# Performance work log

Hardware: AMD Instinct MI355X
Metric: run time of the kernel (lower is better)

## Reference

```python
import jax, jax.numpy as jnp
import numpy as np

NUM_HEADS = 16
FIELD_SIZE = 512
SIGMA = 3.0
EMB = 1024


def _causal_kernel_fft(G, sigma):
    # kernel[i] = exp(-|i - G//2| / sigma) for i < G//2, else 0; normalized
    i = np.arange(G)
    dist = np.abs(i - G // 2)
    kernel = np.where(i >= G // 2, 0.0, np.exp(-dist / sigma)).astype(np.float32)
    kernel = kernel / (kernel.sum() + 1e-8)
    return jnp.asarray(np.fft.rfft(kernel), dtype=jnp.complex64)


def setup_inputs() -> dict:
    key = jax.random.key(0)
    ks = jax.random.split(key, 9)
    B, N, D = 4, 4096, EMB
    s = 1.0 / np.sqrt(D)
    return {
        "x": jax.random.normal(ks[0], (B, N, D), dtype=jnp.float32),
        "q_w": jax.random.uniform(ks[1], (D, D), minval=-s, maxval=s, dtype=jnp.float32),
        "q_b": jnp.zeros((D,), jnp.float32),
        "k_w": jax.random.uniform(ks[2], (D, D), minval=-s, maxval=s, dtype=jnp.float32),
        "k_b": jnp.zeros((D,), jnp.float32),
        "v_w": jax.random.uniform(ks[3], (D, D), minval=-s, maxval=s, dtype=jnp.float32),
        "v_b": jnp.zeros((D,), jnp.float32),
        "out_w": jax.random.uniform(ks[4], (D, D), minval=-s, maxval=s, dtype=jnp.float32),
        "out_b": jnp.zeros((D,), jnp.float32),
    }


def reference(x, q_w, q_b, k_w, k_b, v_w, v_b, out_w, out_b):
    B, N, D = x.shape
    H, hd, G = NUM_HEADS, D // NUM_HEADS, FIELD_SIZE

    # projections (q is computed in the original but unused downstream)
    q = x @ q_w.T + q_b  # noqa: F841 (faithful to original)
    k = (x @ k_w.T + k_b).reshape(B, N, H, hd).transpose(0, 2, 1, 3)  # (B,H,N,hd)
    v = (x @ v_w.T + v_b).reshape(B, N, H, hd).transpose(0, 2, 1, 3)

    # map sequence positions -> field bins (same for all b, h)
    pos = jnp.arange(N, dtype=jnp.float32) / max(N - 1, 1) * (G - 1)
    field_idx = jnp.clip(pos.astype(jnp.int32), 0, G - 1)  # (N,)

    # weighted values by key magnitude
    k_mag = jnp.linalg.norm(k, axis=-1, keepdims=True)  # (B,H,N,1)
    wv = v * k_mag  # (B,H,N,hd)

    # scatter-add tokens into field bins (vectorized over B,H,hd)
    field = jax.ops.segment_sum(wv.transpose(2, 0, 1, 3), field_idx,
                                num_segments=G)  # (G,B,H,hd)
    field = field.transpose(1, 2, 0, 3)  # (B,H,G,hd)

    # causal convolution along the field via FFT (circular, as in original)
    kfft = _causal_kernel_fft(G, SIGMA)
    f_fft = jnp.fft.rfft(field, n=G, axis=2)
    conv = jnp.fft.irfft(f_fft * kfft[None, None, :, None], n=G, axis=2)

    # gather back to token positions
    out = conv[:, :, field_idx, :]  # (B,H,N,hd)
    out = out.transpose(0, 2, 1, 3).reshape(B, N, D)
    return out @ out_w.T + out_b
```

## Files before the change

### kernel.cpp

```cpp
#include <hip/hip_runtime.h>
#include <hip/hip_bf16.h>

#define NPOS 4096
#define DIM  1024
#define GSZ  512

#define GAS __attribute__((address_space(1)))
#define LAS __attribute__((address_space(3)))

typedef __attribute__((ext_vector_type(8))) short bf16x8;
typedef __attribute__((ext_vector_type(4))) float f32x4;

__device__ __forceinline__ void async_load16(const void* g, void* l) {
  __builtin_amdgcn_global_load_lds((const GAS void*)g, (LAS void*)l, 16, 0, 0);
}

__device__ __forceinline__ int fidx_of(int n) {
  return (int)(((float)n / 4095.0f) * 511.0f);
}

__device__ __forceinline__ float bf2f(unsigned short s) {
  union { unsigned u; float f; } v; v.u = ((unsigned)s) << 16; return v.f;
}

__device__ __forceinline__ void bin_range(int g, int& i0, int& i1) {
  i0 = (g * 4095 + 510) / 511;
  while (i0 > 0 && fidx_of(i0 - 1) >= g) --i0;
  while (i0 < NPOS && fidx_of(i0) < g) ++i0;
  if (g == GSZ - 1) { i1 = NPOS; return; }
  i1 = ((g + 1) * 4095 + 510) / 511;
  while (i1 > 0 && fidx_of(i1 - 1) >= g + 1) --i1;
  while (i1 < NPOS && fidx_of(i1) < g + 1) ++i1;
}

__global__ __launch_bounds__(256) void cast_all(
    const float* __restrict__ x, const float* __restrict__ kw,
    const float* __restrict__ vw, const float* __restrict__ ow,
    __hip_bfloat16* __restrict__ xb, __hip_bfloat16* __restrict__ kvwb,
    __hip_bfloat16* __restrict__ outwb) {
  int blk = blockIdx.x;
  const float* src; __hip_bfloat16* dst; int off;
  if (blk < 16384)      { src = x;  dst = xb;              off = blk; }
  else if (blk < 17408) { src = kw; dst = kvwb;            off = blk - 16384; }
  else if (blk < 18432) { src = vw; dst = kvwb + 1048576;  off = blk - 17408; }
  else                  { src = ow; dst = outwb;           off = blk - 18432; }
  int i = (off * 256 + threadIdx.x) * 4;
  float4 f = *(const float4*)(src + i);
  ushort4 o;
  __hip_bfloat16 t;
  t = __float2bfloat16(f.x); o.x = *(unsigned short*)&t;
  t = __float2bfloat16(f.y); o.y = *(unsigned short*)&t;
  t = __float2bfloat16(f.z); o.z = *(unsigned short*)&t;
  t = __float2bfloat16(f.w); o.w = *(unsigned short*)&t;
  *(ushort4*)(dst + i) = o;
}

__global__ __launch_bounds__(256) void gemm_bt(
    const __hip_bfloat16* __restrict__ A,
    const __hip_bfloat16* __restrict__ B,
    const float* __restrict__ bias0, const float* __restrict__ bias1,
    __hip_bfloat16* __restrict__ C, int N) {
  const int K = 1024;
  __shared__ __align__(16) __hip_bfloat16 As[128 * 32];
  __shared__ __align__(16) __hip_bfloat16 Bs[128 * 32];
  const int tid = threadIdx.x;
  const int bm = blockIdx.x * 128, bn = blockIdx.y * 128;

  const int srow = tid >> 2;
  const int scol = (tid & 3) * 8;
  const __hip_bfloat16* ap0 = A + (size_t)(bm + srow) * K + scol;
  const __hip_bfloat16* ap1 = A + (size_t)(bm + srow + 64) * K + scol;
  const __hip_bfloat16* bp0 = B + (size_t)(bn + srow) * K + scol;
  const __hip_bfloat16* bp1 = B + (size_t)(bn + srow + 64) * K + scol;
  __hip_bfloat16* as0 = &As[srow * 32 + scol];
  __hip_bfloat16* as1 = &As[(srow + 64) * 32 + scol];
  __hip_bfloat16* bs0 = &Bs[srow * 32 + scol];
  __hip_bfloat16* bs1 = &Bs[(srow + 64) * 32 + scol];

  const int wave = tid >> 6, lane = tid & 63;
  const int wm = (wave >> 1) * 64, wn = (wave & 1) * 64;
  const int m16 = lane & 15, quad = lane >> 4;

  f32x4 acc[4][4];
#pragma unroll
  for (int i = 0; i < 4; i++)
#pragma unroll
    for (int j = 0; j < 4; j++) acc[i][j] = (f32x4)0.f;

  for (int k0 = 0; k0 < K; k0 += 32) {
    async_load16(ap0 + k0, as0);
    async_load16(ap1 + k0, as1);
    async_load16(bp0 + k0, bs0);
    async_load16(bp1 + k0, bs1);
    __syncthreads();
    bf16x8 af[4], bfr[4];
#pragma unroll
    for (int mt = 0; mt < 4; mt++)
      af[mt] = *(const bf16x8*)&As[(wm + mt * 16 + m16) * 32 + quad * 8];
#pragma unroll
    for (int nt = 0; nt < 4; nt++)
      bfr[nt] = *(const bf16x8*)&Bs[(wn + nt * 16 + m16) * 32 + quad * 8];
#pragma unroll
    for (int mt = 0; mt < 4; mt++)
#pragma unroll
      for (int nt = 0; nt < 4; nt++)
        acc[mt][nt] = __builtin_amdgcn_mfma_f32_16x16x32_bf16(af[mt], bfr[nt], acc[mt][nt], 0, 0, 0);
    __syncthreads();
  }

#pragma unroll
  for (int mt = 0; mt < 4; mt++) {
#pragma unroll
    for (int nt = 0; nt < 4; nt++) {
      int col = bn + wn + nt * 16 + m16;
      float bv = (col < 1024) ? bias0[col] : bias1[col - 1024];
#pragma unroll
      for (int r = 0; r < 4; r++) {
        int row = bm + wm + mt * 16 + quad * 4 + r;
        C[(size_t)row * N + col] = __float2bfloat16(acc[mt][nt][r] + bv);
      }
    }
  }
}

__global__ __launch_bounds__(256) void gemm_out_bcast(
    const __hip_bfloat16* __restrict__ A,
    const __hip_bfloat16* __restrict__ B,
    const float* __restrict__ bias,
    float* __restrict__ out) {
  const int K = 1024;
  __shared__ __align__(16) __hip_bfloat16 As[64 * 32];
  __shared__ __align__(16) __hip_bfloat16 Bs[128 * 32];
  const int tid = threadIdx.x;
  const int bm = blockIdx.x * 64, bn = blockIdx.y * 128;

  const int srow = tid >> 2;
  const int scol = (tid & 3) * 8;
  const __hip_bfloat16* ap0 = A + (size_t)(bm + srow) * K + scol;
  const __hip_bfloat16* bp0 = B + (size_t)(bn + srow) * K + scol;
  const __hip_bfloat16* bp1 = B + (size_t)(bn + srow + 64) * K + scol;
  __hip_bfloat16* as0 = &As[srow * 32 + scol];
  __hip_bfloat16* bs0 = &Bs[srow * 32 + scol];
  __hip_bfloat16* bs1 = &Bs[(srow + 64) * 32 + scol];

  const int wave = tid >> 6, lane = tid & 63;
  const int wm = (wave >> 1) * 32, wn = (wave & 1) * 64;
  const int m16 = lane & 15, quad = lane >> 4;

  f32x4 acc[2][4];
#pragma unroll
  for (int i = 0; i < 2; i++)
#pragma unroll
    for (int j = 0; j < 4; j++) acc[i][j] = (f32x4)0.f;

  for (int k0 = 0; k0 < K; k0 += 32) {
    async_load16(ap0 + k0, as0);
    async_load16(bp0 + k0, bs0);
    async_load16(bp1 + k0, bs1);
    __syncthreads();
    bf16x8 af[2], bfr[4];
#pragma unroll
    for (int mt = 0; mt < 2; mt++)
      af[mt] = *(const bf16x8*)&As[(wm + mt * 16 + m16) * 32 + quad * 8];
#pragma unroll
    for (int nt = 0; nt < 4; nt++)
      bfr[nt] = *(const bf16x8*)&Bs[(wn + nt * 16 + m16) * 32 + quad * 8];
#pragma unroll
    for (int mt = 0; mt < 2; mt++)
#pragma unroll
      for (int nt = 0; nt < 4; nt++)
        acc[mt][nt] = __builtin_amdgcn_mfma_f32_16x16x32_bf16(af[mt], bfr[nt], acc[mt][nt], 0, 0, 0);
    __syncthreads();
  }

  float bv[4];
#pragma unroll
  for (int nt = 0; nt < 4; nt++) bv[nt] = bias[bn + wn + nt * 16 + m16];

#pragma unroll
  for (int mt = 0; mt < 2; mt++) {
#pragma unroll
    for (int r = 0; r < 4; r++) {
      int row = bm + wm + mt * 16 + quad * 4 + r;
      int b = row >> 9, g = row & (GSZ - 1);
      int i0, i1;
      bin_range(g, i0, i1);
      float v0 = acc[mt][0][r] + bv[0];
      float v1 = acc[mt][1][r] + bv[1];
      float v2 = acc[mt][2][r] + bv[2];
      float v3 = acc[mt][3][r] + bv[3];
      for (int n = i0; n < i1; ++n) {
        float* orow = out + ((size_t)(b * NPOS + n)) * DIM + bn + wn + m16;
        orow[0]  = v0;
        orow[16] = v1;
        orow[32] = v2;
        orow[48] = v3;
      }
    }
  }
}

__global__ __launch_bounds__(256) void wv_field_kernel(
    const __hip_bfloat16* __restrict__ KV, float* __restrict__ field) {
  const int b = blockIdx.x, g = blockIdx.y;
  int i0, i1;
  bin_range(g, i0, i1);
  int cnt = i1 - i0;
  if (cnt > 12) cnt = 12;
  __shared__ float km[12][16];
  const int tid = threadIdx.x;
  if (tid < cnt * 16) {
    int r = tid >> 4, h = tid & 15;
    const unsigned short* kp = (const unsigned short*)KV + (size_t)(b * NPOS + i0 + r) * 2048 + h * 64;
    float s = 0.f;
#pragma unroll
    for (int e = 0; e < 64; e += 8) {
      bf16x8 v = *(const bf16x8*)(kp + e);
#pragma unroll
      for (int q = 0; q < 8; ++q) { float f = bf2f((unsigned short)v[q]); s += f * f; }
    }
    km[r][h] = sqrtf(s);
  }
  __syncthreads();
  if (tid < 128) {
    int c0 = tid * 8, h = c0 >> 6;
    float acc[8] = {0.f, 0.f, 0.f, 0.f, 0.f, 0.f, 0.f, 0.f};
    for (int r = 0; r < cnt; ++r) {
      float w = km[r][h];
      bf16x8 v = *(const bf16x8*)((const unsigned short*)KV + (size_t)(b * NPOS + i0 + r) * 2048 + 1024 + c0);
#pragma unroll
      for (int q = 0; q < 8; ++q) acc[q] += w * bf2f((unsigned short)v[q]);
    }
    float4* fp = (float4*)(field + ((size_t)(b * GSZ + g)) * DIM + c0);
    fp[0] = make_float4(acc[0], acc[1], acc[2], acc[3]);
    fp[1] = make_float4(acc[4], acc[5], acc[6], acc[7]);
  }
}

__global__ __launch_bounds__(256) void conv_ema_kernel(
    const float* __restrict__ field, __hip_bfloat16* __restrict__ convb) {
  const int b = blockIdx.x, h = blockIdx.y;
  const int tid = threadIdx.x;
  const int c = tid & 63;
  const int chunk = blockIdx.z * 4 + (tid >> 6);
  const int n0 = chunk * 64;
  const float a = expf(-1.0f / 3.0f);
  const float w1 = 1.0f - a;
  const float* fb = field + (size_t)b * GSZ * DIM + h * 64 + c;
  float acc = 0.f;
#pragma unroll 4
  for (int n = n0 + 127; n >= n0 + 64; --n) {
    float f = fb[(size_t)((n + 257) & (GSZ - 1)) * DIM];
    acc = w1 * f + a * acc;
  }
#pragma unroll 4
  for (int n = n0 + 63; n >= n0; --n) {
    float f = fb[(size_t)((n + 257) & (GSZ - 1)) * DIM];
    acc = w1 * f + a * acc;
    convb[((size_t)(b * GSZ) + n) * DIM + h * 64 + c] = __float2bfloat16(acc);
  }
}

extern "C" void kernel_launch(void* const* d_in, const int* in_sizes, int n_in,
                              void* d_out, int out_size, void* d_ws, size_t ws_size,
                              hipStream_t stream) {
  (void)in_sizes; (void)n_in; (void)out_size; (void)ws_size;
  const float* x     = (const float*)d_in[0];
  const float* k_w   = (const float*)d_in[3];
  const float* k_b   = (const float*)d_in[4];
  const float* v_w   = (const float*)d_in[5];
  const float* v_b   = (const float*)d_in[6];
  const float* out_w = (const float*)d_in[7];
  const float* out_b = (const float*)d_in[8];

  char* p = (char*)d_ws;
  __hip_bfloat16* xb    = (__hip_bfloat16*)p; p += (size_t)16384 * 1024 * 2;
  __hip_bfloat16* kvwb  = (__hip_bfloat16*)p; p += (size_t)2048 * 1024 * 2;
  __hip_bfloat16* outwb = (__hip_bfloat16*)p; p += (size_t)1024 * 1024 * 2;
  __hip_bfloat16* KV    = (__hip_bfloat16*)p; p += (size_t)16384 * 2048 * 2;
  float*          field = (float*)p;          p += (size_t)4 * 512 * 1024 * 4;
  __hip_bfloat16* convb = (__hip_bfloat16*)p;

  cast_all<<<19456, 256, 0, stream>>>(x, k_w, v_w, out_w, xb, kvwb, outwb);

  gemm_bt<<<dim3(128, 16), 256, 0, stream>>>(xb, kvwb, k_b, v_b, KV, 2048);

  wv_field_kernel<<<dim3(4, 512), 256, 0, stream>>>(KV, field);
  conv_ema_kernel<<<dim3(4, 16, 2), 256, 0, stream>>>(field, convb);

  gemm_out_bcast<<<dim3(32, 8), 256, 0, stream>>>(convb, outwb, out_b, (float*)d_out);
}
```

Measured before the change: 283.5 us.

## Stage conv field slab in LDS and coalesce broadcast output writes via LDS

The causal EMA convolution kernel now loads a 192-row slab of the field into shared memory with float4 loads and runs its recurrence from LDS. The grid doubles to 128-row chunks, each using 64 rows of warm-up per 32-row sub-chunk. The output GEMM stages its result tile in LDS and then writes each broadcast output row with fully coalesced float4 stores, where it previously issued strided scalar stores per MFMA lane. This targets the write bandwidth of the large 64MB output, at the cost of extra LDS traffic and a barrier.

```diff
diff --git a/kernel.cpp b/kernel.cpp
--- a/kernel.cpp
+++ b/kernel.cpp
@@ -123,14 +123,80 @@
   }
 }
 
+__global__ __launch_bounds__(256) void wv_field_kernel(
+    const __hip_bfloat16* __restrict__ KV, float* __restrict__ field) {
+  const int b = blockIdx.x, g = blockIdx.y;
+  int i0, i1;
+  bin_range(g, i0, i1);
+  int cnt = i1 - i0;
+  if (cnt > 12) cnt = 12;
+  __shared__ float km[12][16];
+  const int tid = threadIdx.x;
+  if (tid < cnt * 16) {
+    int r = tid >> 4, h = tid & 15;
+    const unsigned short* kp = (const unsigned short*)KV + (size_t)(b * NPOS + i0 + r) * 2048 + h * 64;
+    float s = 0.f;
+#pragma unroll
+    for (int e = 0; e < 64; e += 8) {
+      bf16x8 v = *(const bf16x8*)(kp + e);
+#pragma unroll
+      for (int q = 0; q < 8; ++q) { float f = bf2f((unsigned short)v[q]); s += f * f; }
+    }
+    km[r][h] = sqrtf(s);
+  }
+  __syncthreads();
+  if (tid < 128) {
+    int c0 = tid * 8, h = c0 >> 6;
+    float acc[8] = {0.f, 0.f, 0.f, 0.f, 0.f, 0.f, 0.f, 0.f};
+    for (int r = 0; r < cnt; ++r) {
+      float w = km[r][h];
+      bf16x8 v = *(const bf16x8*)((const unsigned short*)KV + (size_t)(b * NPOS + i0 + r) * 2048 + 1024 + c0);
+#pragma unroll
+      for (int q = 0; q < 8; ++q) acc[q] += w * bf2f((unsigned short)v[q]);
+    }
+    float4* fp = (float4*)(field + ((size_t)(b * GSZ + g)) * DIM + c0);
+    fp[0] = make_float4(acc[0], acc[1], acc[2], acc[3]);
+    fp[1] = make_float4(acc[4], acc[5], acc[6], acc[7]);
+  }
+}
+
+__global__ __launch_bounds__(256) void conv_ema_kernel(
+    const float* __restrict__ field, __hip_bfloat16* __restrict__ convb) {
+  const int b = blockIdx.x, h = blockIdx.y, n0 = blockIdx.z * 128;
+  __shared__ float slab[192 * 64];
+  const int tid = threadIdx.x;
+  const float* fb = field + (size_t)b * GSZ * DIM + h * 64;
+  for (int i = tid; i < 192 * 16; i += 256) {
+    int row = i >> 4, c4 = i & 15;
+    int gg = (n0 + 257 + row) & (GSZ - 1);
+    *(float4*)&slab[row * 64 + c4 * 4] = *(const float4*)(fb + (size_t)gg * DIM + c4 * 4);
+  }
+  __syncthreads();
+  const float a = 0.71653131057378927f;
+  const float w1 = 1.0f - a;
+  const int c = tid & 63, sub = tid >> 6;
+  const int e0 = sub * 32;
+  float acc = 0.f;
+#pragma unroll 4
+  for (int t = e0 + 95; t >= e0 + 32; --t)
+    acc = w1 * slab[t * 64 + c] + a * acc;
+#pragma unroll
+  for (int t = e0 + 31; t >= e0; --t) {
+    acc = w1 * slab[t * 64 + c] + a * acc;
+    convb[((size_t)(b * GSZ) + n0 + t) * DIM + h * 64 + c] = __float2bfloat16(acc);
+  }
+}
+
 __global__ __launch_bounds__(256) void gemm_out_bcast(
     const __hip_bfloat16* __restrict__ A,
     const __hip_bfloat16* __restrict__ B,
     const float* __restrict__ bias,
     float* __restrict__ out) {
   const int K = 1024;
-  __shared__ __align__(16) __hip_bfloat16 As[64 * 32];
-  __shared__ __align__(16) __hip_bfloat16 Bs[128 * 32];
+  __shared__ __align__(16) char lds[64 * 132 * 4];
+  __hip_bfloat16* As = (__hip_bfloat16*)lds;
+  __hip_bfloat16* Bs = (__hip_bfloat16*)(lds + 4096);
+  float* Ct = (float*)lds;
   const int tid = threadIdx.x;
   const int bm = blockIdx.x * 64, bn = blockIdx.y * 128;
 
@@ -173,91 +239,32 @@
     __syncthreads();
   }
 
-  float bv[4];
-#pragma unroll
-  for (int nt = 0; nt < 4; nt++) bv[nt] = bias[bn + wn + nt * 16 + m16];
-
 #pragma unroll
   for (int mt = 0; mt < 2; mt++) {
 #pragma unroll
-    for (int r = 0; r < 4; r++) {
-      int row = bm + wm + mt * 16 + quad * 4 + r;
-      int b = row >> 9, g = row & (GSZ - 1);
-      int i0, i1;
-      bin_range(g, i0, i1);
-      float v0 = acc[mt][0][r] + bv[0];
-      float v1 = acc[mt][1][r] + bv[1];
-      float v2 = acc[mt][2][r] + bv[2];
-      float v3 = acc[mt][3][r] + bv[3];
-      for (int n = i0; n < i1; ++n) {
-        float* orow = out + ((size_t)(b * NPOS + n)) * DIM + bn + wn + m16;
-        orow[0]  = v0;
-        orow[16] = v1;
-        orow[32] = v2;
-        orow[48] = v3;
+    for (int nt = 0; nt < 4; nt++) {
+      int col = wn + nt * 16 + m16;
+      float bv = bias[bn + col];
+#pragma unroll
+      for (int r = 0; r < 4; r++) {
+        int row = wm + mt * 16 + quad * 4 + r;
+        Ct[row * 132 + col] = acc[mt][nt][r] + bv;
       }
     }
   }
-}
-
-__global__ __launch_bounds__(256) void wv_field_kernel(
-    const __hip_bfloat16* __restrict__ KV, float* __restrict__ field) {
-  const int b = blockIdx.x, g = blockIdx.y;
-  int i0, i1;
-  bin_range(g, i0, i1);
-  int cnt = i1 - i0;
-  if (cnt > 12) cnt = 12;
-  __shared__ float km[12][16];
-  const int tid = threadIdx.x;
-  if (tid < cnt * 16) {
-    int r = tid >> 4, h = tid & 15;
-    const unsigned short* kp = (const unsigned short*)KV + (size_t)(b * NPOS + i0 + r) * 2048 + h * 64;
-    float s = 0.f;
-#pragma unroll
-    for (int e = 0; e < 64; e += 8) {
-      bf16x8 v = *(const bf16x8*)(kp + e);
-#pragma unroll
-      for (int q = 0; q < 8; ++q) { float f = bf2f((unsigned short)v[q]); s += f * f; }
-    }
-    km[r][h] = sqrtf(s);
-  }
   __syncthreads();
-  if (tid < 128) {
-    int c0 = tid * 8, h = c0 >> 6;
-    float acc[8] = {0.f, 0.f, 0.f, 0.f, 0.f, 0.f, 0.f, 0.f};
-    for (int r = 0; r < cnt; ++r) {
-      float w = km[r][h];
-      bf16x8 v = *(const bf16x8*)((const unsigned short*)KV + (size_t)(b * NPOS + i0 + r) * 2048 + 1024 + c0);
-#pragma unroll
-      for (int q = 0; q < 8; ++q) acc[q] += w * bf2f((unsigned short)v[q]);
-    }
-    float4* fp = (float4*)(field + ((size_t)(b * GSZ + g)) * DIM + c0);
-    fp[0] = make_float4(acc[0], acc[1], acc[2], acc[3]);
-    fp[1] = make_float4(acc[4], acc[5], acc[6], acc[7]);
-  }
-}
-
-__global__ __launch_bounds__(256) void conv_ema_kernel(
-    const float* __restrict__ field, __hip_bfloat16* __restrict__ convb) {
-  const int b = blockIdx.x, h = blockIdx.y;
-  const int tid = threadIdx.x;
-  const int c = tid & 63;
-  const int chunk = blockIdx.z * 4 + (tid >> 6);
-  const int n0 = chunk * 64;
-  const float a = expf(-1.0f / 3.0f);
-  const float w1 = 1.0f - a;
-  const float* fb = field + (size_t)b * GSZ * DIM + h * 64 + c;
-  float acc = 0.f;
-#pragma unroll 4
-  for (int n = n0 + 127; n >= n0 + 64; --n) {
-    float f = fb[(size_t)((n + 257) & (GSZ - 1)) * DIM];
-    acc = w1 * f + a * acc;
-  }
-#pragma unroll 4
-  for (int n = n0 + 63; n >= n0; --n) {
-    float f = fb[(size_t)((n + 257) & (GSZ - 1)) * DIM];
-    acc = w1 * f + a * acc;
-    convb[((size_t)(b * GSZ) + n) * DIM + h * 64 + c] = __float2bfloat16(acc);
+
+  for (int gi = 0; gi < 64; ++gi) {
+    int R = bm + gi;
+    int b = R >> 9, g = R & (GSZ - 1);
+    int i0, i1;
+    bin_range(g, i0, i1);
+    int cnt = i1 - i0;
+    const float4* src = (const float4*)&Ct[gi * 132];
+    for (int it = tid; it < cnt * 32; it += 256) {
+      int n = i0 + (it >> 5), c4 = it & 31;
+      *(float4*)(out + ((size_t)(b * NPOS + n)) * DIM + bn + c4 * 4) = src[c4];
+    }
   }
 }
 
@@ -286,7 +293,7 @@
   gemm_bt<<<dim3(128, 16), 256, 0, stream>>>(xb, kvwb, k_b, v_b, KV, 2048);
 
   wv_field_kernel<<<dim3(4, 512), 256, 0, stream>>>(KV, field);
-  conv_ema_kernel<<<dim3(4, 16, 2), 256, 0, stream>>>(field, convb);
+  conv_ema_kernel<<<dim3(4, 16, 4), 256, 0, stream>>>(field, convb);
 
   gemm_out_bcast<<<dim3(32, 8), 256, 0, stream>>>(convb, outwb, out_b, (float*)d_out);
 }
```

After: 345.5 us. +21.9%, slower.
